# Performance work log

Measured on AMD Instinct MI355X. Metric: run time of the kernel, lower is better.

## Reference

```python
import jax, jax.numpy as jnp
import numpy as np

DIM = 768
HEADS = 12
HEAD_DIM = DIM // HEADS
HIDDEN = int(DIM * 1.0)  # mlp_ratio = 1.0
EPS = 1e-5


def layer_norm(x, g, b):
    mu = jnp.mean(x, axis=-1, keepdims=True)
    var = jnp.mean(jnp.square(x - mu), axis=-1, keepdims=True)
    return (x - mu) * jax.lax.rsqrt(var + EPS) * g + b


def setup_inputs() -> dict:
    key = jax.random.key(0)
    ks = jax.random.split(key, 8)
    s = 0.02
    return {
        "x": jax.random.normal(ks[0], (8, 1024, DIM), dtype=jnp.float32),
        "mask": jnp.ones((8, 1024), dtype=jnp.int32),
        "g1": jnp.ones((DIM,), jnp.float32),
        "b1": jnp.zeros((DIM,), jnp.float32),
        "w_qkv": jax.random.normal(ks[1], (DIM, 3 * DIM), jnp.float32) * s,
        "w_proj": jax.random.normal(ks[2], (DIM, DIM), jnp.float32) * s,
        "b_proj": jnp.zeros((DIM,), jnp.float32),
        "g2": jnp.ones((DIM,), jnp.float32),
        "b2": jnp.zeros((DIM,), jnp.float32),
        "w_fc1": jax.random.normal(ks[3], (DIM, HIDDEN), jnp.float32) * s,
        "b_fc1": jnp.zeros((HIDDEN,), jnp.float32),
        "w_fc2": jax.random.normal(ks[4], (HIDDEN, DIM), jnp.float32) * s,
        "b_fc2": jnp.zeros((DIM,), jnp.float32),
    }


def reference(x, mask, g1, b1, w_qkv, w_proj, b_proj, g2, b2, w_fc1, b_fc1, w_fc2, b_fc2):
    B, N, C = x.shape
    scale = HEAD_DIM ** -0.5

    # --- attention (pre-norm) ---
    h = layer_norm(x, g1, b1)
    qkv = (h @ w_qkv).reshape(B, N, 3, HEADS, HEAD_DIM)
    qkv = jnp.transpose(qkv, (2, 0, 3, 1, 4))  # 3, b, h, n, d
    q, k, v = qkv[0], qkv[1], qkv[2]

    attn = jnp.einsum("bhnd,bhmd->bhnm", q, k) * scale
    # mask: (B, N) -> pairwise mask (B, 1, N, N)
    pair = (mask[:, None, :, None] * mask[:, None, None, :]) != 0
    attn = jnp.where(pair, attn, jnp.float32(-1e9))
    attn = jax.nn.softmax(attn, axis=-1)

    o = jnp.einsum("bhnm,bhmd->bhnd", attn, v)
    o = jnp.transpose(o, (0, 2, 1, 3)).reshape(B, N, C)
    o = o @ w_proj + b_proj
    x = x + o

    # --- MLP (pre-norm) ---
    h2 = layer_norm(x, g2, b2)
    h2 = jax.nn.gelu(h2 @ w_fc1 + b_fc1, approximate=False)
    h2 = h2 @ w_fc2 + b_fc2
    return x + h2
```

## Files before the change

### kernel.cpp

```cpp
#include <hip/hip_runtime.h>
#include <stdint.h>
#include <math.h>

using short8 = __attribute__((ext_vector_type(8))) short;
using f32x4  = __attribute__((ext_vector_type(4))) float;

#define DEV __device__ __forceinline__
#define S_VMCNT(n) asm volatile("s_waitcnt vmcnt(" #n ")" ::: "memory")
#define S_LGKM(n)  asm volatile("s_waitcnt lgkmcnt(" #n ")" ::: "memory")
#define S_LGKM0()  asm volatile("s_waitcnt lgkmcnt(0)" ::: "memory")
#define SCHED0()   __builtin_amdgcn_sched_barrier(0)
#define SBAR()     __builtin_amdgcn_s_barrier()

DEV unsigned short f2bf(float f) {
    union { float f; unsigned u; } c; c.f = f;
    unsigned u = c.u;
    unsigned r = (u + 0x7FFFu + ((u >> 16) & 1u)) >> 16;
    return (unsigned short)r;
}

DEV float bf2f(unsigned short h) {
    union { unsigned u; float f; } c; c.u = ((unsigned)h) << 16;
    return c.f;
}

DEV void gld16(const unsigned short* g, unsigned short* l) {
    __builtin_amdgcn_global_load_lds(
        (const __attribute__((address_space(1))) void*)g,
        (__attribute__((address_space(3))) void*)l, 16, 0, 0);
}

DEV unsigned ldsaddr(unsigned short* p) {
    return (unsigned)(uintptr_t)(__attribute__((address_space(3))) unsigned short*)p;
}

DEV unsigned cvtpk(float lo, float hi) {
    unsigned r;
    asm("v_cvt_pk_bf16_f32 %0, %1, %2" : "=v"(r) : "v"(lo), "v"(hi));
    return r;
}

DEV uint2 tr16(unsigned addr) {
    uint2 r;
    asm volatile("ds_read_b64_tr_b16 %0, %1" : "=v"(r) : "v"(addr));
    return r;
}

__global__ __launch_bounds__(256) void k_transpose_all(
    const float* __restrict__ w0, const float* __restrict__ w1,
    const float* __restrict__ w2, const float* __restrict__ w3,
    unsigned short* __restrict__ o0, unsigned short* __restrict__ o1,
    unsigned short* __restrict__ o2, unsigned short* __restrict__ o3)
{
    __shared__ float tile[32][33];
    int z = blockIdx.z;
    const float* W = (z == 0) ? w0 : (z == 1) ? w1 : (z == 2) ? w2 : w3;
    unsigned short* Wt = (z == 0) ? o0 : (z == 1) ? o1 : (z == 2) ? o2 : o3;
    int N = (z == 0) ? 2304 : 768;
    int n0 = blockIdx.x * 32, k0 = blockIdx.y * 32;
    if (n0 >= N) return;
    int tx = threadIdx.x, ty = threadIdx.y;
#pragma unroll
    for (int i = 0; i < 4; i++) {
        int k = k0 + ty + i * 8;
        tile[ty + i * 8][tx] = W[(size_t)k * N + n0 + tx];
    }
    __syncthreads();
#pragma unroll
    for (int i = 0; i < 4; i++) {
        int n = n0 + ty + i * 8;
        Wt[(size_t)n * 768 + k0 + tx] = f2bf(tile[tx][ty + i * 8]);
    }
}

template<int BF>
__global__ __launch_bounds__(256) void k_layernorm(
    const void* __restrict__ xin, const float* __restrict__ g,
    const float* __restrict__ b, unsigned short* __restrict__ out)
{
    int row = blockIdx.x;
    int tid = threadIdx.x;
    float v0, v1, v2;
    if (BF) {
        const unsigned short* xr = (const unsigned short*)xin + (size_t)row * 768;
        v0 = bf2f(xr[tid]); v1 = bf2f(xr[tid + 256]); v2 = bf2f(xr[tid + 512]);
    } else {
        const float* xr = (const float*)xin + (size_t)row * 768;
        v0 = xr[tid]; v1 = xr[tid + 256]; v2 = xr[tid + 512];
    }
    float s1 = v0 + v1 + v2;
    float s2 = v0 * v0 + v1 * v1 + v2 * v2;
#pragma unroll
    for (int off = 32; off >= 1; off >>= 1) {
        s1 += __shfl_down(s1, off);
        s2 += __shfl_down(s2, off);
    }
    __shared__ float red[8];
    int wid = tid >> 6, lane = tid & 63;
    if (lane == 0) { red[wid] = s1; red[4 + wid] = s2; }
    __syncthreads();
    s1 = red[0] + red[1] + red[2] + red[3];
    s2 = red[4] + red[5] + red[6] + red[7];
    float mu = s1 * (1.0f / 768.0f);
    float var = s2 * (1.0f / 768.0f) - mu * mu;
    float rs = rsqrtf(var + 1e-5f);
    unsigned short* orow = out + (size_t)row * 768;
    orow[tid]       = f2bf((v0 - mu) * rs * g[tid]       + b[tid]);
    orow[tid + 256] = f2bf((v1 - mu) * rs * g[tid + 256] + b[tid + 256]);
    orow[tid + 512] = f2bf((v2 - mu) * rs * g[tid + 512] + b[tid + 512]);
}

template<int EPI, int BN>
__global__ __launch_bounds__(256) void k_gemm(
    const unsigned short* __restrict__ A, const unsigned short* __restrict__ Bt,
    const float* __restrict__ bias,
    const float* __restrict__ residF, const unsigned short* __restrict__ residH,
    float* __restrict__ outF, unsigned short* __restrict__ outH,
    unsigned short* __restrict__ qb, unsigned short* __restrict__ kb,
    unsigned short* __restrict__ vtb)
{
    constexpr int KK = 768, NK = 12;
    constexpr int MI = (BN == 128) ? 4 : 2;
    constexpr int NJ = 4;
    __shared__ __align__(16) unsigned short As[2][128 * 64];
    __shared__ __align__(16) unsigned short Bs[2][BN * 64];

    int tid = threadIdx.x;
    int lane = tid & 63, wid = tid >> 6;

    int gy = gridDim.y;
    int nwg = 64 * gy;
    int bid = blockIdx.x + blockIdx.y * 64;
    int nid = (bid & 7) * (nwg >> 3) + (bid >> 3);
    int bx = nid / gy;
    int by = nid - bx * gy;
    int m0 = bx * 128, n0 = by * BN;

    int wr = (BN == 128) ? (wid >> 1) * 64 : wid * 32;
    int wc = (BN == 128) ? (wid & 1) * 64 : 0;
    int fr = lane & 15, fg = lane >> 4;
    int fr7 = fr & 7;

    f32x4 zero4 = {0.f, 0.f, 0.f, 0.f};
    f32x4 acc[MI][NJ];
#pragma unroll
    for (int mi = 0; mi < MI; mi++)
#pragma unroll
        for (int nj = 0; nj < NJ; nj++) acc[mi][nj] = zero4;

    int srow = wid * 8 + (lane >> 3);
    int schk = (lane & 7) ^ (lane >> 3);
    const unsigned short* ga = A  + (size_t)(m0 + srow) * KK + schk * 8;
    const unsigned short* gb = Bt + (size_t)(n0 + srow) * KK + schk * 8;

    auto stage = [&](int kt, int s) {
        int ko = kt * 64;
#pragma unroll
        for (int i = 0; i < 4; i++)
            gld16(ga + (size_t)i * 32 * KK + ko, As[s] + i * 2048 + wid * 512);
#pragma unroll
        for (int i = 0; i < BN / 32; i++)
            gld16(gb + (size_t)i * 32 * KK + ko, Bs[s] + i * 2048 + wid * 512);
    };

    int aoff0 = (wr + fr) * 64;
    int boff0 = (wc + fr) * 64;

    stage(0, 0);

    for (int k = 0; k < NK; ++k) {
        if (k + 1 < NK) {
            stage(k + 1, (k + 1) & 1);
            if constexpr (BN == 128) { S_VMCNT(8); } else { S_VMCNT(6); }
        } else {
            S_VMCNT(0);
        }
        SCHED0(); SBAR(); SCHED0();

        const unsigned short* Ac = As[k & 1];
        const unsigned short* Bc = Bs[k & 1];
#pragma unroll
        for (int kk = 0; kk < 2; ++kk) {
            int off = (((kk << 2) | fg) ^ fr7) * 8;
            short8 af[MI], bfv[NJ];
#pragma unroll
            for (int mi = 0; mi < MI; mi++)
                af[mi] = *(const short8*)(Ac + aoff0 + mi * 1024 + off);
#pragma unroll
            for (int nj = 0; nj < NJ; nj++)
                bfv[nj] = *(const short8*)(Bc + boff0 + nj * 1024 + off);
#pragma unroll
            for (int mi = 0; mi < MI; mi++)
#pragma unroll
                for (int nj = 0; nj < NJ; nj++)
                    acc[mi][nj] = __builtin_amdgcn_mfma_f32_16x16x32_bf16(
                        af[mi], bfv[nj], acc[mi][nj], 0, 0, 0);
        }
        SCHED0(); SBAR(); SCHED0();
    }

#pragma unroll
    for (int mi = 0; mi < MI; mi++) {
#pragma unroll
        for (int nj = 0; nj < NJ; nj++) {
#pragma unroll
            for (int i = 0; i < 4; i++) {
                int grow = m0 + wr + mi * 16 + fg * 4 + i;
                int gcol = n0 + wc + nj * 16 + fr;
                float v = acc[mi][nj][i];
                if (EPI == 0) {
                    int part = gcol / 768;
                    int wi = gcol - part * 768;
                    int head = wi >> 6, d = wi & 63;
                    int bb = grow >> 10, n = grow & 1023;
                    size_t base = ((size_t)(bb * 12 + head)) << 16;
                    unsigned short bv = f2bf(v);
                    if (part == 0)      qb[base + (size_t)n * 64 + d] = bv;
                    else if (part == 1) kb[base + (size_t)n * 64 + d] = bv;
                    else                vtb[base + (size_t)d * 1024 + n] = bv;
                } else if (EPI == 1) {
                    size_t idx = (size_t)grow * 768 + gcol;
                    outH[idx] = f2bf(v + bias[gcol] + residF[idx]);
                } else if (EPI == 2) {
                    float t = v + bias[gcol];
                    outH[(size_t)grow * 768 + gcol] =
                        f2bf(0.5f * t * (1.0f + erff(t * 0.70710678118f)));
                } else {
                    size_t idx = (size_t)grow * 768 + gcol;
                    outF[idx] = v + bias[gcol] + bf2f(residH[idx]);
                }
            }
        }
    }
}

__global__ __launch_bounds__(512) void k_attn(
    const unsigned short* __restrict__ Q, const unsigned short* __restrict__ Kk,
    const unsigned short* __restrict__ Vt, const int* __restrict__ mask,
    unsigned short* __restrict__ O)
{
    __shared__ __align__(16) unsigned short KsA[3 * 4096];
    __shared__ __align__(16) unsigned short VsA[3 * 4096];
    __shared__ __align__(16) unsigned short PT[8 * 1024];
    __shared__ float mskf[1024];

    int tid = threadIdx.x, lane = tid & 63, wid = tid >> 6;
    int bid = blockIdx.x + blockIdx.y * 8;
    int nid = (bid & 7) * 96 + (bid >> 3);
    int qt = nid & 7;
    int bh = nid >> 3;
    int b = bh / 12;
    int hh = bh - b * 12;
    int fr = lane & 15, fg = lane >> 4;

    const unsigned short* qg = Q  + ((size_t)bh << 16);
    const unsigned short* kg = Kk + ((size_t)bh << 16);
    const unsigned short* vg = Vt + ((size_t)bh << 16);

    for (int i = tid; i < 1024; i += 512)
        mskf[i] = mask[b * 1024 + i] ? 1.f : 0.f;

    short8 qf[2];
    {
        const unsigned short* qp = qg + (size_t)(qt * 128 + wid * 16 + fr) * 64 + fg * 8;
        qf[0] = *(const short8*)(qp);
        qf[1] = *(const short8*)(qp + 32);
    }

    int srow = wid * 8 + (lane >> 3);
    int schk = (lane & 7) ^ ((lane >> 3) & 7);
    const unsigned short* kgp = kg + (size_t)srow * 64 + schk * 8;
    const unsigned short* vgp = vg + (size_t)srow * 1024 + schk * 8;

    auto stage = [&](int kn, int s) {
        gld16(kgp + (size_t)(kn * 64) * 64, &KsA[s * 4096] + wid * 512);
        gld16(vgp + kn * 64, &VsA[s * 4096] + wid * 512);
    };

    stage(0, 0);
    __syncthreads();

    f32x4 zero4 = {0.f, 0.f, 0.f, 0.f};
    f32x4 oacc[4];
    f32x4 lacc = zero4;
#pragma unroll
    for (int df = 0; df < 4; df++) oacc[df] = zero4;

    short8 ones8;
#pragma unroll
    for (int j = 0; j < 8; j++) ones8[j] = (short)0x3F80;

    const float SC = 0.125f * 1.44269504f;

    unsigned short* pw = &PT[wid * 1024];
    unsigned trbase = ldsaddr(pw) + fg * 256 + fr * 2;

    int pos0 = fg ^ (fr & 7);
    int pos1 = (fg + 4) ^ (fr & 7);

#pragma unroll
    for (int kc = 0; kc < 16; ++kc) {
        S_VMCNT(0);
        SCHED0(); SBAR(); SCHED0();
        if (kc < 15) { stage(kc + 1, (kc + 1) % 3); SCHED0(); }

        const unsigned short* Kc = &KsA[(kc % 3) * 4096];
        short8 kb0[4], kb1[4];
#pragma unroll
        for (int nf = 0; nf < 4; ++nf) {
            int row = nf * 16 + fr;
            kb0[nf] = *(const short8*)(Kc + row * 64 + pos0 * 8);
            kb1[nf] = *(const short8*)(Kc + row * 64 + pos1 * 8);
        }
        SCHED0();

        f32x4 s[4];
        if (kc > 0) {
            S_LGKM(8);
            uint2 r00 = tr16(trbase);
            uint2 r01 = tr16(trbase + 128);
            uint2 r10 = tr16(trbase + 1024);
            uint2 r11 = tr16(trbase + 1024 + 128);
            S_LGKM(4);
            SCHED0();
            __builtin_amdgcn_s_setprio(1);
#pragma unroll
            for (int nf = 0; nf < 4; ++nf) {
                f32x4 a = zero4;
                a = __builtin_amdgcn_mfma_f32_16x16x32_bf16(qf[0], kb0[nf], a, 0, 0, 0);
                a = __builtin_amdgcn_mfma_f32_16x16x32_bf16(qf[1], kb1[nf], a, 0, 0, 0);
                s[nf] = a;
            }
            __builtin_amdgcn_s_setprio(0);

            const unsigned short* Vp = &VsA[(((kc - 1) % 3)) * 4096];
            short8 vb0[4], vb1[4];
#pragma unroll
            for (int df = 0; df < 4; ++df) {
                int rv = df * 16 + fr;
                vb0[df] = *(const short8*)(Vp + rv * 64 + pos0 * 8);
                vb1[df] = *(const short8*)(Vp + rv * 64 + pos1 * 8);
            }

            union { unsigned u[4]; short8 s8; } pa0, pa1;
            pa0.u[0] = r00.x; pa0.u[1] = r00.y; pa0.u[2] = r01.x; pa0.u[3] = r01.y;
            pa1.u[0] = r10.x; pa1.u[1] = r10.y; pa1.u[2] = r11.x; pa1.u[3] = r11.y;

            uint2 w[4];
#pragma unroll
            for (int nf = 0; nf < 4; nf++) {
                float mk = mskf[kc * 64 + nf * 16 + fr];
                float p0 = __builtin_amdgcn_exp2f(s[nf][0] * SC) * mk;
                float p1 = __builtin_amdgcn_exp2f(s[nf][1] * SC) * mk;
                float p2 = __builtin_amdgcn_exp2f(s[nf][2] * SC) * mk;
                float p3 = __builtin_amdgcn_exp2f(s[nf][3] * SC) * mk;
                w[nf].x = cvtpk(p0, p1); w[nf].y = cvtpk(p2, p3);
            }

            S_LGKM0();
            SCHED0();
            __builtin_amdgcn_s_setprio(1);
#pragma unroll
            for (int df = 0; df < 4; df++) {
                oacc[df] = __builtin_amdgcn_mfma_f32_16x16x32_bf16(pa0.s8, vb0[df], oacc[df], 0, 0, 0);
                oacc[df] = __builtin_amdgcn_mfma_f32_16x16x32_bf16(pa1.s8, vb1[df], oacc[df], 0, 0, 0);
            }
            lacc = __builtin_amdgcn_mfma_f32_16x16x32_bf16(pa0.s8, ones8, lacc, 0, 0, 0);
            lacc = __builtin_amdgcn_mfma_f32_16x16x32_bf16(pa1.s8, ones8, lacc, 0, 0, 0);
            __builtin_amdgcn_s_setprio(0);

#pragma unroll
            for (int nf = 0; nf < 4; nf++)
                *(uint2*)(pw + (nf * 16 + fr) * 16 + fg * 4) = w[nf];
        } else {
            S_LGKM0();
            SCHED0();
            __builtin_amdgcn_s_setprio(1);
#pragma unroll
            for (int nf = 0; nf < 4; ++nf) {
                f32x4 a = zero4;
                a = __builtin_amdgcn_mfma_f32_16x16x32_bf16(qf[0], kb0[nf], a, 0, 0, 0);
                a = __builtin_amdgcn_mfma_f32_16x16x32_bf16(qf[1], kb1[nf], a, 0, 0, 0);
                s[nf] = a;
            }
            __builtin_amdgcn_s_setprio(0);
#pragma unroll
            for (int nf = 0; nf < 4; nf++) {
                float mk = mskf[nf * 16 + fr];
                float p0 = __builtin_amdgcn_exp2f(s[nf][0] * SC) * mk;
                float p1 = __builtin_amdgcn_exp2f(s[nf][1] * SC) * mk;
                float p2 = __builtin_amdgcn_exp2f(s[nf][2] * SC) * mk;
                float p3 = __builtin_amdgcn_exp2f(s[nf][3] * SC) * mk;
                uint2 w0; w0.x = cvtpk(p0, p1); w0.y = cvtpk(p2, p3);
                *(uint2*)(pw + (nf * 16 + fr) * 16 + fg * 4) = w0;
            }
        }
    }

    {
        uint2 r00 = tr16(trbase);
        uint2 r01 = tr16(trbase + 128);
        uint2 r10 = tr16(trbase + 1024);
        uint2 r11 = tr16(trbase + 1024 + 128);
        const unsigned short* Vp = &VsA[0];
        short8 vb0[4], vb1[4];
#pragma unroll
        for (int df = 0; df < 4; ++df) {
            int rv = df * 16 + fr;
            vb0[df] = *(const short8*)(Vp + rv * 64 + pos0 * 8);
            vb1[df] = *(const short8*)(Vp + rv * 64 + pos1 * 8);
        }
        S_LGKM0(); SCHED0();
        union { unsigned u[4]; short8 s8; } pa0, pa1;
        pa0.u[0] = r00.x; pa0.u[1] = r00.y; pa0.u[2] = r01.x; pa0.u[3] = r01.y;
        pa1.u[0] = r10.x; pa1.u[1] = r10.y; pa1.u[2] = r11.x; pa1.u[3] = r11.y;
#pragma unroll
        for (int df = 0; df < 4; df++) {
            oacc[df] = __builtin_amdgcn_mfma_f32_16x16x32_bf16(pa0.s8, vb0[df], oacc[df], 0, 0, 0);
            oacc[df] = __builtin_amdgcn_mfma_f32_16x16x32_bf16(pa1.s8, vb1[df], oacc[df], 0, 0, 0);
        }
        lacc = __builtin_amdgcn_mfma_f32_16x16x32_bf16(pa0.s8, ones8, lacc, 0, 0, 0);
        lacc = __builtin_amdgcn_mfma_f32_16x16x32_bf16(pa1.s8, ones8, lacc, 0, 0, 0);
    }

#pragma unroll
    for (int i = 0; i < 4; i++) {
        float inv = 1.0f / fmaxf(lacc[i], 1e-30f);
        size_t rowbase = ((size_t)(b * 1024 + qt * 128 + wid * 16 + fg * 4 + i)) * 768
                         + hh * 64 + fr;
#pragma unroll
        for (int df = 0; df < 4; df++)
            O[rowbase + df * 16] = f2bf(oacc[df][i] * inv);
    }
}

extern "C" void kernel_launch(void* const* d_in, const int* in_sizes, int n_in,
                              void* d_out, int out_size, void* d_ws, size_t ws_size,
                              hipStream_t stream)
{
    const float* x      = (const float*)d_in[0];
    const int*   mask   = (const int*)d_in[1];
    const float* g1     = (const float*)d_in[2];
    const float* b1     = (const float*)d_in[3];
    const float* w_qkv  = (const float*)d_in[4];
    const float* w_proj = (const float*)d_in[5];
    const float* b_proj = (const float*)d_in[6];
    const float* g2     = (const float*)d_in[7];
    const float* b2     = (const float*)d_in[8];
    const float* w_fc1  = (const float*)d_in[9];
    const float* b_fc1  = (const float*)d_in[10];
    const float* w_fc2  = (const float*)d_in[11];
    const float* b_fc2  = (const float*)d_in[12];
    float* out = (float*)d_out;

    char* ws = (char*)d_ws;
    unsigned short* wqkv_t  = (unsigned short*)(ws + 0);
    unsigned short* wproj_t = (unsigned short*)(ws + 3538944);
    unsigned short* wfc1_t  = (unsigned short*)(ws + 4718592);
    unsigned short* wfc2_t  = (unsigned short*)(ws + 5898240);
    unsigned short* bufA    = (unsigned short*)(ws + 7077888);
    unsigned short* bufB    = (unsigned short*)(ws + 19660800);
    unsigned short* qb      = (unsigned short*)(ws + 32243712);
    unsigned short* kb      = (unsigned short*)(ws + 44826624);
    unsigned short* vtb     = (unsigned short*)(ws + 57409536);
    unsigned short* x1b     = (unsigned short*)(ws + 69992448);

    k_transpose_all<<<dim3(72, 24, 4), dim3(32, 8), 0, stream>>>(
        w_qkv, w_proj, w_fc1, w_fc2, wqkv_t, wproj_t, wfc1_t, wfc2_t);

    k_layernorm<0><<<8192, 256, 0, stream>>>(x, g1, b1, bufA);

    k_gemm<0, 128><<<dim3(64, 18), 256, 0, stream>>>(bufA, wqkv_t,
        nullptr, nullptr, nullptr, nullptr, nullptr, qb, kb, vtb);

    k_attn<<<dim3(8, 96), 512, 0, stream>>>(qb, kb, vtb, mask, bufB);

    k_gemm<1, 64><<<dim3(64, 12), 256, 0, stream>>>(bufB, wproj_t,
        b_proj, x, nullptr, nullptr, x1b, nullptr, nullptr, nullptr);

    k_layernorm<1><<<8192, 256, 0, stream>>>(x1b, g2, b2, bufA);

    k_gemm<2, 64><<<dim3(64, 12), 256, 0, stream>>>(bufA, wfc1_t,
        b_fc1, nullptr, nullptr, nullptr, bufB, nullptr, nullptr, nullptr);

    k_gemm<3, 64><<<dim3(64, 12), 256, 0, stream>>>(bufB, wfc2_t,
        b_fc2, nullptr, x1b, out, nullptr, nullptr, nullptr, nullptr);
}
```

Before: 176.8 us.

## Add 8-wave 256x128 QKV GEMM kernel with triple-buffered interleaved pipeline

Replaces the QKV projection GEMM with a dedicated 512-thread kernel that uses 256x128 tiles and a three-stage LDS ring. Global loads for tile t+2 and LDS fragment reads are interleaved with the MFMA blocks, with s_setprio raised around the MFMAs. The aim is to hide load latency and raise MFMA utilization on the largest GEMM. The cost is more LDS (144KB) and register pressure, plus fewer workgroups (576) and more barriers per k-step. The generic GEMM template is simplified to BN=64 only.

New measurement: 183.7 us (median of 2 runs). 1.04x slower.

```diff
diff --git a/kernel.cpp b/kernel.cpp
--- a/kernel.cpp
+++ b/kernel.cpp
@@ -110,18 +110,162 @@
     orow[tid + 512] = f2bf((v2 - mu) * rs * g[tid + 512] + b[tid + 512]);
 }
 
-template<int EPI, int BN>
+__global__ __launch_bounds__(512) void k_gemm8(
+    const unsigned short* __restrict__ A, const unsigned short* __restrict__ Bt,
+    unsigned short* __restrict__ qb, unsigned short* __restrict__ kb,
+    unsigned short* __restrict__ vtb)
+{
+    constexpr int KK = 768;
+    __shared__ __align__(16) unsigned short As[3 * 256 * 64];
+    __shared__ __align__(16) unsigned short Bs[3 * 128 * 64];
+
+    int tid = threadIdx.x, lane = tid & 63, wid = tid >> 6;
+
+    int bid = blockIdx.x + blockIdx.y * 32;
+    int nid = (bid & 7) * 72 + (bid >> 3);
+    int bx = nid / 18;
+    int by = nid - bx * 18;
+    int m0 = bx * 256, n0 = by * 128;
+
+    int wr = (wid >> 1) * 64, wc = (wid & 1) * 64;
+    int fr = lane & 15, fg = lane >> 4;
+    int fr7 = fr & 7;
+
+    f32x4 zero4 = {0.f, 0.f, 0.f, 0.f};
+    f32x4 acc[4][4];
+#pragma unroll
+    for (int mi = 0; mi < 4; mi++)
+#pragma unroll
+        for (int nj = 0; nj < 4; nj++) acc[mi][nj] = zero4;
+
+    int srow = tid >> 3;
+    int schk = (tid & 7) ^ ((tid >> 3) & 7);
+    const unsigned short* ga = A  + (size_t)(m0 + srow) * KK + schk * 8;
+    const unsigned short* gb = Bt + (size_t)(n0 + srow) * KK + schk * 8;
+
+    auto stageA = [&](int t, int h) {
+        unsigned short* d = As + (t % 3) * 16384 + h * 8192 + wid * 512;
+        int ko = t * 64;
+        gld16(ga + (size_t)(h * 128) * KK + ko, d);
+        gld16(ga + (size_t)(h * 128 + 64) * KK + ko, d + 4096);
+    };
+    auto stageB = [&](int t) {
+        unsigned short* d = Bs + (t % 3) * 8192 + wid * 512;
+        int ko = t * 64;
+        gld16(gb + ko, d);
+        gld16(gb + (size_t)64 * KK + ko, d + 4096);
+    };
+    auto AF = [&](int mi, int kk, int t) -> short8 {
+        return *(const short8*)(As + (t % 3) * 16384 +
+            (wr + mi * 16 + fr) * 64 + ((((kk << 2) | fg) ^ fr7) << 3));
+    };
+    auto BF = [&](int nj, int kk, int t) -> short8 {
+        return *(const short8*)(Bs + (t % 3) * 8192 +
+            (wc + nj * 16 + fr) * 64 + ((((kk << 2) | fg) ^ fr7) << 3));
+    };
+
+    stageA(0, 0); stageA(0, 1); stageB(0);
+    stageA(1, 0); stageA(1, 1); stageB(1);
+    S_VMCNT(6);
+    SCHED0(); SBAR(); SCHED0();
+
+    short8 aA = AF(0, 0, 0), aB = AF(1, 0, 0);
+    short8 bk0[4], bk1[4];
+#pragma unroll
+    for (int nj = 0; nj < 4; nj++) bk0[nj] = BF(nj, 0, 0);
+
+#pragma unroll
+    for (int t = 0; t < 12; ++t) {
+        if (t + 2 < 12) stageA(t + 2, 0);
+        short8 aC = AF(2, 0, t), aD = AF(3, 0, t);
+        SCHED0(); SBAR();
+        S_LGKM(2); SCHED0();
+        __builtin_amdgcn_s_setprio(1);
+#pragma unroll
+        for (int nj = 0; nj < 4; nj++) {
+            acc[0][nj] = __builtin_amdgcn_mfma_f32_16x16x32_bf16(aA, bk0[nj], acc[0][nj], 0, 0, 0);
+            acc[1][nj] = __builtin_amdgcn_mfma_f32_16x16x32_bf16(aB, bk0[nj], acc[1][nj], 0, 0, 0);
+        }
+        __builtin_amdgcn_s_setprio(0);
+
+        if (t + 2 < 12) stageA(t + 2, 1);
+        short8 aE = AF(0, 1, t), aF = AF(1, 1, t);
+#pragma unroll
+        for (int nj = 0; nj < 4; nj++) bk1[nj] = BF(nj, 1, t);
+        SCHED0(); SBAR();
+        S_LGKM(6); SCHED0();
+        __builtin_amdgcn_s_setprio(1);
+#pragma unroll
+        for (int nj = 0; nj < 4; nj++) {
+            acc[2][nj] = __builtin_amdgcn_mfma_f32_16x16x32_bf16(aC, bk0[nj], acc[2][nj], 0, 0, 0);
+            acc[3][nj] = __builtin_amdgcn_mfma_f32_16x16x32_bf16(aD, bk0[nj], acc[3][nj], 0, 0, 0);
+        }
+        __builtin_amdgcn_s_setprio(0);
+
+        if (t + 2 < 12) stageB(t + 2);
+        short8 aG = AF(2, 1, t), aH = AF(3, 1, t);
+        SCHED0(); SBAR();
+        S_LGKM(2); SCHED0();
+        __builtin_amdgcn_s_setprio(1);
+#pragma unroll
+        for (int nj = 0; nj < 4; nj++) {
+            acc[0][nj] = __builtin_amdgcn_mfma_f32_16x16x32_bf16(aE, bk1[nj], acc[0][nj], 0, 0, 0);
+            acc[1][nj] = __builtin_amdgcn_mfma_f32_16x16x32_bf16(aF, bk1[nj], acc[1][nj], 0, 0, 0);
+        }
+        __builtin_amdgcn_s_setprio(0);
+
+        if (t + 1 < 12) {
+            if (t + 2 < 12) { S_VMCNT(6); } else { S_VMCNT(0); }
+            SCHED0(); SBAR(); SCHED0();
+            aA = AF(0, 0, t + 1); aB = AF(1, 0, t + 1);
+#pragma unroll
+            for (int nj = 0; nj < 4; nj++) bk0[nj] = BF(nj, 0, t + 1);
+            S_LGKM(6); SCHED0();
+        } else {
+            SCHED0(); SBAR();
+            S_LGKM0(); SCHED0();
+        }
+        __builtin_amdgcn_s_setprio(1);
+#pragma unroll
+        for (int nj = 0; nj < 4; nj++) {
+            acc[2][nj] = __builtin_amdgcn_mfma_f32_16x16x32_bf16(aG, bk1[nj], acc[2][nj], 0, 0, 0);
+            acc[3][nj] = __builtin_amdgcn_mfma_f32_16x16x32_bf16(aH, bk1[nj], acc[3][nj], 0, 0, 0);
+        }
+        __builtin_amdgcn_s_setprio(0);
+    }
+
+#pragma unroll
+    for (int mi = 0; mi < 4; mi++) {
+#pragma unroll
+        for (int nj = 0; nj < 4; nj++) {
+#pragma unroll
+            for (int i = 0; i < 4; i++) {
+                int grow = m0 + wr + mi * 16 + fg * 4 + i;
+                int gcol = n0 + wc + nj * 16 + fr;
+                float v = acc[mi][nj][i];
+                int part = gcol / 768;
+                int wi = gcol - part * 768;
+                int head = wi >> 6, d = wi & 63;
+                int bb = grow >> 10, n = grow & 1023;
+                size_t base = ((size_t)(bb * 12 + head)) << 16;
+                unsigned short bv = f2bf(v);
+                if (part == 0)      qb[base + (size_t)n * 64 + d] = bv;
+                else if (part == 1) kb[base + (size_t)n * 64 + d] = bv;
+                else                vtb[base + (size_t)d * 1024 + n] = bv;
+            }
+        }
+    }
+}
+
+template<int EPI>
 __global__ __launch_bounds__(256) void k_gemm(
     const unsigned short* __restrict__ A, const unsigned short* __restrict__ Bt,
     const float* __restrict__ bias,
     const float* __restrict__ residF, const unsigned short* __restrict__ residH,
-    float* __restrict__ outF, unsigned short* __restrict__ outH,
-    unsigned short* __restrict__ qb, unsigned short* __restrict__ kb,
-    unsigned short* __restrict__ vtb)
+    float* __restrict__ outF, unsigned short* __restrict__ outH)
 {
-    constexpr int KK = 768, NK = 12;
-    constexpr int MI = (BN == 128) ? 4 : 2;
-    constexpr int NJ = 4;
+    constexpr int KK = 768, NK = 12, BN = 64;
+    constexpr int MI = 2, NJ = 4;
     __shared__ __align__(16) unsigned short As[2][128 * 64];
     __shared__ __align__(16) unsigned short Bs[2][BN * 64];
 
@@ -136,8 +280,7 @@
     int by = nid - bx * gy;
     int m0 = bx * 128, n0 = by * BN;
 
-    int wr = (BN == 128) ? (wid >> 1) * 64 : wid * 32;
-    int wc = (BN == 128) ? (wid & 1) * 64 : 0;
+    int wr = wid * 32, wc = 0;
     int fr = lane & 15, fg = lane >> 4;
     int fr7 = fr & 7;
 
@@ -159,7 +302,7 @@
         for (int i = 0; i < 4; i++)
             gld16(ga + (size_t)i * 32 * KK + ko, As[s] + i * 2048 + wid * 512);
 #pragma unroll
-        for (int i = 0; i < BN / 32; i++)
+        for (int i = 0; i < 2; i++)
             gld16(gb + (size_t)i * 32 * KK + ko, Bs[s] + i * 2048 + wid * 512);
     };
 
@@ -171,7 +314,7 @@
     for (int k = 0; k < NK; ++k) {
         if (k + 1 < NK) {
             stage(k + 1, (k + 1) & 1);
-            if constexpr (BN == 128) { S_VMCNT(8); } else { S_VMCNT(6); }
+            S_VMCNT(6);
         } else {
             S_VMCNT(0);
         }
@@ -208,17 +351,7 @@
                 int grow = m0 + wr + mi * 16 + fg * 4 + i;
                 int gcol = n0 + wc + nj * 16 + fr;
                 float v = acc[mi][nj][i];
-                if (EPI == 0) {
-                    int part = gcol / 768;
-                    int wi = gcol - part * 768;
-                    int head = wi >> 6, d = wi & 63;
-                    int bb = grow >> 10, n = grow & 1023;
-                    size_t base = ((size_t)(bb * 12 + head)) << 16;
-                    unsigned short bv = f2bf(v);
-                    if (part == 0)      qb[base + (size_t)n * 64 + d] = bv;
-                    else if (part == 1) kb[base + (size_t)n * 64 + d] = bv;
-                    else                vtb[base + (size_t)d * 1024 + n] = bv;
-                } else if (EPI == 1) {
+                if (EPI == 1) {
                     size_t idx = (size_t)grow * 768 + gcol;
                     outH[idx] = f2bf(v + bias[gcol] + residF[idx]);
                 } else if (EPI == 2) {
@@ -470,19 +603,18 @@
 
     k_layernorm<0><<<8192, 256, 0, stream>>>(x, g1, b1, bufA);
 
-    k_gemm<0, 128><<<dim3(64, 18), 256, 0, stream>>>(bufA, wqkv_t,
-        nullptr, nullptr, nullptr, nullptr, nullptr, qb, kb, vtb);
+    k_gemm8<<<dim3(32, 18), 512, 0, stream>>>(bufA, wqkv_t, qb, kb, vtb);
 
     k_attn<<<dim3(8, 96), 512, 0, stream>>>(qb, kb, vtb, mask, bufB);
 
-    k_gemm<1, 64><<<dim3(64, 12), 256, 0, stream>>>(bufB, wproj_t,
-        b_proj, x, nullptr, nullptr, x1b, nullptr, nullptr, nullptr);
+    k_gemm<1><<<dim3(64, 12), 256, 0, stream>>>(bufB, wproj_t,
+        b_proj, x, nullptr, nullptr, x1b);
 
     k_layernorm<1><<<8192, 256, 0, stream>>>(x1b, g2, b2, bufA);
 
-    k_gemm<2, 64><<<dim3(64, 12), 256, 0, stream>>>(bufA, wfc1_t,
-        b_fc1, nullptr, nullptr, nullptr, bufB, nullptr, nullptr, nullptr);
-
-    k_gemm<3, 64><<<dim3(64, 12), 256, 0, stream>>>(bufB, wfc2_t,
-        b_fc2, nullptr, x1b, out, nullptr, nullptr, nullptr, nullptr);
-}
+    k_gemm<2><<<dim3(64, 12), 256, 0, stream>>>(bufA, wfc1_t,
+        b_fc1, nullptr, nullptr, nullptr, bufB);
+
+    k_gemm<3><<<dim3(64, 12), 256, 0, stream>>>(bufB, wfc2_t,
+        b_fc2, nullptr, x1b, out, nullptr);
+}
```
